# Optimization experiments

Hardware: AMD Instinct MI355X
Metric: run time of the kernel (lower is better)

The kernel has to match this reference:

```python
import jax, jax.numpy as jnp
import numpy as np

BN_EPS = 1e-5
NUM_GC_LAYERS = 3
NUM_LAYERS = NUM_GC_LAYERS + 4  # 7
N_NODES = 50000
N_EDGES = 600000
DIM = 128


def setup_inputs() -> dict:
    key = jax.random.key(0)
    ks = jax.random.split(key, 9)
    x = jax.random.normal(ks[0], (N_NODES, DIM), dtype=jnp.float32)
    edge_index = jax.random.randint(ks[1], (2, N_EDGES), 0, N_NODES, dtype=jnp.int64)
    batch = jnp.zeros((N_NODES,), dtype=jnp.int64)
    s = 0.1
    W1 = jax.random.normal(ks[2], (NUM_LAYERS, DIM, DIM), dtype=jnp.float32) * s
    b1 = jax.random.normal(ks[3], (NUM_LAYERS, DIM), dtype=jnp.float32) * s
    W2 = jax.random.normal(ks[4], (NUM_LAYERS, DIM, DIM), dtype=jnp.float32) * s
    b2 = jax.random.normal(ks[5], (NUM_LAYERS, DIM), dtype=jnp.float32) * s
    gamma = jnp.ones((NUM_LAYERS, DIM), dtype=jnp.float32)
    beta = jnp.zeros((NUM_LAYERS, DIM), dtype=jnp.float32)
    return {"x": x, "edge_index": edge_index, "batch": batch,
            "W1": W1, "b1": b1, "W2": W2, "b2": b2,
            "gamma": gamma, "beta": beta}


def _gin_conv(x, src, dst, W1, b1, W2, b2):
    # GINConv with eps=0: out = MLP(x + sum_{j in N(i)} x_j)
    agg = jax.ops.segment_sum(x[src], dst, num_segments=x.shape[0])  # [N, D]
    h = x + agg
    h = jnp.maximum(h @ W1 + b1, 0.0) @ W2 + b2
    return h


def _batch_norm(h, g, b):
    # BatchNorm1d in training mode: biased batch stats over nodes
    mean = jnp.mean(h, axis=0)
    var = jnp.var(h, axis=0)
    return (h - mean) * jax.lax.rsqrt(var + BN_EPS) * g + b


def reference(x, edge_index, batch, W1, b1, W2, b2, gamma, beta):
    src, dst = edge_index[0], edge_index[1]
    for i in range(NUM_GC_LAYERS):
        h = _gin_conv(x, src, dst, W1[i], b1[i], W2[i], b2[i])
        x = _batch_norm(jnp.maximum(h, 0.0), gamma[i], beta[i])
    j = NUM_GC_LAYERS
    outs = []
    for k in range(j, j + 4):
        h = _gin_conv(x, src, dst, W1[k], b1[k], W2[k], b2[k])
        outs.append(_batch_norm(jnp.tanh(h), gamma[k], beta[k]))
    return tuple(outs)
```

## Files before the change

### kernel.cpp

```cpp
#include <hip/hip_runtime.h>
#include <math.h>

#define NN 50000
#define NE 600000
#define DIM 128
#define NLAYERS 7
#define LDK 136
#define BN_EPS 1e-5f
#define GB 782
#define PART_SLOT 200192

typedef __attribute__((ext_vector_type(4))) float floatx4;
typedef __attribute__((ext_vector_type(8))) _Float16 half8;
typedef __attribute__((ext_vector_type(2))) _Float16 half2v;

__device__ __forceinline__ unsigned short f2h(float f) {
  _Float16 h = (_Float16)f;
  return __builtin_bit_cast(unsigned short, h);
}
__device__ __forceinline__ float2 up(unsigned int u) {
  half2v h = __builtin_bit_cast(half2v, u);
  return make_float2((float)h.x, (float)h.y);
}
__device__ __forceinline__ unsigned int pk(float a, float b) {
  half2v h;
  h.x = (_Float16)a;
  h.y = (_Float16)b;
  return __builtin_bit_cast(unsigned int, h);
}


__global__ void hist_kernel(const int* __restrict__ ei, int* __restrict__ deg) {
  int e = blockIdx.x * 256 + threadIdx.x;
  if (e < NE) atomicAdd(&deg[ei[NE + e]], 1);
}

__global__ __launch_bounds__(256) void scan_part(const int* __restrict__ deg,
                                                 int* __restrict__ rowl,
                                                 int* __restrict__ bsum) {
  int b = blockIdx.x, t = threadIdx.x;
  int base = b * 1024 + t * 4;
  int d[4];
  #pragma unroll
  for (int j = 0; j < 4; j++) d[j] = (base + j < NN) ? deg[base + j] : 0;
  int s = d[0] + d[1] + d[2] + d[3];
  int lane = t & 63;
  int incl = s;
  #pragma unroll
  for (int off = 1; off < 64; off <<= 1) {
    int n = __shfl_up(incl, off);
    if (lane >= off) incl += n;
  }
  __shared__ int wtot[4];
  if (lane == 63) wtot[t >> 6] = incl;
  __syncthreads();
  int woff = 0;
  for (int w = 0; w < (t >> 6); w++) woff += wtot[w];
  int run = woff + incl - s;
  #pragma unroll
  for (int j = 0; j < 4; j++) {
    if (base + j < NN) rowl[base + j] = run;
    run += d[j];
  }
  if (t == 255) bsum[b] = woff + incl;
}

__global__ void scan_top(const int* __restrict__ bsum, int* __restrict__ boff,
                         int* __restrict__ row) {
  int t = threadIdx.x;
  int v = (t < 49) ? bsum[t] : 0;
  int incl = v;
  #pragma unroll
  for (int off = 1; off < 64; off <<= 1) {
    int n = __shfl_up(incl, off);
    if (t >= off) incl += n;
  }
  if (t < 49) boff[t] = incl - v;
  if (t == 48) row[NN] = incl;
}

__global__ __launch_bounds__(256) void scan_apply(const int* __restrict__ rowl,
                                                  const int* __restrict__ boff,
                                                  int* __restrict__ row,
                                                  int* __restrict__ cur) {
  int i = blockIdx.x * 256 + threadIdx.x;
  if (i < NN) {
    int r = rowl[i] + boff[i >> 10];
    row[i] = r;
    cur[i] = r;
  }
}

__global__ void bucket_kernel(const int* __restrict__ ei, int* __restrict__ cur,
                              int* __restrict__ esrc) {
  int e = blockIdx.x * 256 + threadIdx.x;
  if (e < NE) {
    int d = ei[NE + e];
    int p = atomicAdd(&cur[d], 1);
    esrc[p] = ei[e];
  }
}


__global__ void convw_kernel(const float* __restrict__ W1, const float* __restrict__ W2,
                             unsigned short* __restrict__ wb) {
  int i = blockIdx.x * 256 + threadIdx.x;
  if (i >= NLAYERS * 16384) return;
  int l = i >> 14;
  int r = i & 16383;
  int n = r >> 7;
  int k = r & 127;
  wb[(size_t)(l * 2 + 0) * 16384 + n * 128 + k] = f2h(W1[(size_t)l * 16384 + k * 128 + n]);
  wb[(size_t)(l * 2 + 1) * 16384 + n * 128 + k] = f2h(W2[(size_t)l * 16384 + k * 128 + n]);
}

__global__ __launch_bounds__(256) void convx_kernel(const float* __restrict__ x,
                                                    unsigned int* __restrict__ x16) {
  int i = blockIdx.x * 256 + threadIdx.x;
  float4 v = ((const float4*)x)[i];
  uint2 o;
  o.x = pk(v.x, v.y);
  o.y = pk(v.z, v.w);
  ((uint2*)x16)[i] = o;
}


__global__ __launch_bounds__(256) void gather_kernel(
    const unsigned int* __restrict__ x16, const int* __restrict__ esrc,
    const int* __restrict__ row, unsigned int* __restrict__ agg16) {
  int w = (blockIdx.x * 256 + threadIdx.x) >> 6;
  int lane = threadIdx.x & 63;
  if (w >= NN) return;
  int s0 = row[w], s1 = row[w + 1];
  float ax = 0.f, ay = 0.f;
  int e = s0;
  for (; e + 3 < s1; e += 4) {
    int i0 = esrc[e], i1 = esrc[e + 1], i2 = esrc[e + 2], i3 = esrc[e + 3];
    unsigned int v0 = x16[i0 * 64 + lane];
    unsigned int v1 = x16[i1 * 64 + lane];
    unsigned int v2 = x16[i2 * 64 + lane];
    unsigned int v3 = x16[i3 * 64 + lane];
    float2 f0 = up(v0), f1 = up(v1), f2 = up(v2), f3 = up(v3);
    ax += (f0.x + f1.x) + (f2.x + f3.x);
    ay += (f0.y + f1.y) + (f2.y + f3.y);
  }
  for (; e < s1; e++) {
    float2 f = up(x16[esrc[e] * 64 + lane]);
    ax += f.x;
    ay += f.y;
  }
  agg16[w * 64 + lane] = pk(ax, ay);
}


__global__ __launch_bounds__(256) void mlp1_kernel(
    const unsigned int* __restrict__ x16, const unsigned int* __restrict__ agg16,
    const unsigned short* __restrict__ wb,
    const float* __restrict__ b1, const float* __restrict__ b2,
    unsigned short* __restrict__ xout16, float* __restrict__ part,
    const float* __restrict__ bnPrev, const float* __restrict__ gPrev,
    const float* __restrict__ btPrev, const int* __restrict__ deg, int hasPrev) {
  __shared__ unsigned short hS[64 * LDK];
  __shared__ unsigned short wS[128 * LDK];
  __shared__ float scshS[256];
  int tid = threadIdx.x;
  int row0 = blockIdx.x * 64;

  if (tid < 128) {
    float sc = 1.f, sh = 0.f;
    if (hasPrev) {
      const float inv = 1.f / (float)NN;
      float mean = bnPrev[tid] * inv;
      float var = bnPrev[128 + tid] * inv - mean * mean;
      sc = gPrev[tid] * rsqrtf(var + BN_EPS);
      sh = btPrev[tid] - mean * sc;
    }
    scshS[tid] = sc;
    scshS[128 + tid] = sh;
  }
  __syncthreads();

  for (int idx = tid; idx < 1024; idx += 256) {
    int r = idx >> 4;
    int c = (idx & 15) * 8;
    uint4 hv = {0u, 0u, 0u, 0u};
    if (row0 + r < NN) {
      size_t base = (size_t)(row0 + r) * 16 + (c >> 3);
      uint4 xv = ((const uint4*)x16)[base];
      uint4 av = ((const uint4*)agg16)[base];
      float dr = 1.f + (float)deg[row0 + r];
      unsigned int xs[4] = {xv.x, xv.y, xv.z, xv.w};
      unsigned int as_[4] = {av.x, av.y, av.z, av.w};
      unsigned int hs[4];
      #pragma unroll
      for (int j = 0; j < 4; j++) {
        float2 xf = up(xs[j]);
        float2 af = up(as_[j]);
        int cc = c + j * 2;
        float h0 = scshS[cc] * (xf.x + af.x) + dr * scshS[128 + cc];
        float h1 = scshS[cc + 1] * (xf.y + af.y) + dr * scshS[128 + cc + 1];
        hs[j] = pk(h0, h1);
      }
      hv.x = hs[0]; hv.y = hs[1]; hv.z = hs[2]; hv.w = hs[3];
    }
    *(uint4*)&hS[r * LDK + c] = hv;
  }
  for (int q = tid; q < 2048; q += 256) {
    int rw = q >> 4;
    int c8 = (q & 15) * 8;
    *(uint4*)&wS[rw * LDK + c8] = *(const uint4*)(wb + rw * 128 + c8);
  }
  __syncthreads();

  int lane = tid & 63;
  int wav = tid >> 6;
  int quad = lane >> 4;
  int lm = lane & 15;
  int mrow = wav * 16 + lm;

  floatx4 acc[8];
  #pragma unroll
  for (int nt = 0; nt < 8; nt++) {
    floatx4 c = {0.f, 0.f, 0.f, 0.f};
    #pragma unroll
    for (int ks = 0; ks < 4; ks++) {
      half8 af = *(half8*)&hS[mrow * LDK + ks * 32 + quad * 8];
      half8 bf = *(half8*)&wS[(nt * 16 + lm) * LDK + ks * 32 + quad * 8];
      c = __builtin_amdgcn_mfma_f32_16x16x32_f16(af, bf, c, 0, 0, 0);
    }
    acc[nt] = c;
  }
  #pragma unroll
  for (int nt = 0; nt < 8; nt++) {
    float bv = b1[nt * 16 + lm];
    #pragma unroll
    for (int rg = 0; rg < 4; rg++) {
      float v = acc[nt][rg] + bv;
      v = v > 0.f ? v : 0.f;
      hS[(wav * 16 + quad * 4 + rg) * LDK + nt * 16 + lm] = f2h(v);
    }
  }
  __syncthreads();
  for (int q = tid; q < 2048; q += 256) {
    int rw = q >> 4;
    int c8 = (q & 15) * 8;
    *(uint4*)&wS[rw * LDK + c8] = *(const uint4*)(wb + 16384 + rw * 128 + c8);
  }
  __syncthreads();

  bool wvalid = (row0 + wav * 16) < NN;
  float sArr[8], sqArr[8];
  #pragma unroll
  for (int nt = 0; nt < 8; nt++) {
    floatx4 c = {0.f, 0.f, 0.f, 0.f};
    #pragma unroll
    for (int ks = 0; ks < 4; ks++) {
      half8 af = *(half8*)&hS[mrow * LDK + ks * 32 + quad * 8];
      half8 bf = *(half8*)&wS[(nt * 16 + lm) * LDK + ks * 32 + quad * 8];
      c = __builtin_amdgcn_mfma_f32_16x16x32_f16(af, bf, c, 0, 0, 0);
    }
    float bv = b2[nt * 16 + lm];
    float s = 0.f, sq = 0.f;
    #pragma unroll
    for (int rg = 0; rg < 4; rg++) {
      float v = c[rg] + bv;
      v = v > 0.f ? v : 0.f;
      if (wvalid)
        xout16[(size_t)(row0 + wav * 16 + quad * 4 + rg) * DIM + nt * 16 + lm] = f2h(v);
      s += v;
      sq += v * v;
    }
    s += __shfl_xor(s, 16);
    s += __shfl_xor(s, 32);
    sq += __shfl_xor(sq, 16);
    sq += __shfl_xor(sq, 32);
    sArr[nt] = s;
    sqArr[nt] = sq;
  }
  __syncthreads();
  float* redS = (float*)hS;
  if (quad == 0) {
    #pragma unroll
    for (int nt = 0; nt < 8; nt++) {
      redS[wav * 256 + nt * 16 + lm] = wvalid ? sArr[nt] : 0.f;
      redS[wav * 256 + 128 + nt * 16 + lm] = wvalid ? sqArr[nt] : 0.f;
    }
  }
  __syncthreads();
  float v = redS[tid] + redS[256 + tid] + redS[512 + tid] + redS[768 + tid];
  part[(size_t)blockIdx.x * 256 + tid] = v;
}


__global__ __launch_bounds__(256) void mlp4_kernel(
    const unsigned int* __restrict__ x16, const unsigned int* __restrict__ agg16,
    const unsigned short* __restrict__ wbg,
    const float* __restrict__ b1g, const float* __restrict__ b2g,
    float* __restrict__ out, float* __restrict__ partBase,
    const float* __restrict__ bnPrev, const float* __restrict__ gPrev,
    const float* __restrict__ btPrev, const int* __restrict__ deg) {
  __shared__ unsigned short hS[64 * LDK];
  __shared__ unsigned short wS[128 * LDK];
  __shared__ float scshS[256];
  int tid = threadIdx.x;
  int row0 = blockIdx.x * 64;

  if (tid < 128) {
    const float inv = 1.f / (float)NN;
    float mean = bnPrev[tid] * inv;
    float var = bnPrev[128 + tid] * inv - mean * mean;
    float sc = gPrev[tid] * rsqrtf(var + BN_EPS);
    scshS[tid] = sc;
    scshS[128 + tid] = btPrev[tid] - mean * sc;
  }
  __syncthreads();

  for (int idx = tid; idx < 1024; idx += 256) {
    int r = idx >> 4;
    int c = (idx & 15) * 8;
    uint4 hv = {0u, 0u, 0u, 0u};
    if (row0 + r < NN) {
      size_t base = (size_t)(row0 + r) * 16 + (c >> 3);
      uint4 xv = ((const uint4*)x16)[base];
      uint4 av = ((const uint4*)agg16)[base];
      float dr = 1.f + (float)deg[row0 + r];
      unsigned int xs[4] = {xv.x, xv.y, xv.z, xv.w};
      unsigned int as_[4] = {av.x, av.y, av.z, av.w};
      unsigned int hs[4];
      #pragma unroll
      for (int j = 0; j < 4; j++) {
        float2 xf = up(xs[j]);
        float2 af = up(as_[j]);
        int cc = c + j * 2;
        float h0 = scshS[cc] * (xf.x + af.x) + dr * scshS[128 + cc];
        float h1 = scshS[cc + 1] * (xf.y + af.y) + dr * scshS[128 + cc + 1];
        hs[j] = pk(h0, h1);
      }
      hv.x = hs[0]; hv.y = hs[1]; hv.z = hs[2]; hv.w = hs[3];
    }
    *(uint4*)&hS[r * LDK + c] = hv;
  }
  __syncthreads();

  int lane = tid & 63;
  int wav = tid >> 6;
  int quad = lane >> 4;
  int lm = lane & 15;
  int mrow = wav * 16 + lm;
  bool wvalid = (row0 + wav * 16) < NN;

  half8 aF[4];
  #pragma unroll
  for (int ks = 0; ks < 4; ks++)
    aF[ks] = *(half8*)&hS[mrow * LDK + ks * 32 + quad * 8];

  #pragma unroll 1
  for (int ly = 0; ly < 4; ly++) {
    int layer = 3 + ly;
    const unsigned short* wb = wbg + (size_t)layer * 2 * 16384;
    const float* b1 = b1g + layer * 128;
    const float* b2 = b2g + layer * 128;
    float* act = out + (size_t)ly * NN * DIM;
    float* part = partBase + (size_t)ly * PART_SLOT;

    __syncthreads();
    for (int q = tid; q < 2048; q += 256) {
      int rw = q >> 4;
      int c8 = (q & 15) * 8;
      *(uint4*)&wS[rw * LDK + c8] = *(const uint4*)(wb + rw * 128 + c8);
    }
    __syncthreads();

    floatx4 acc[8];
    #pragma unroll
    for (int nt = 0; nt < 8; nt++) {
      floatx4 c = {0.f, 0.f, 0.f, 0.f};
      #pragma unroll
      for (int ks = 0; ks < 4; ks++) {
        half8 bf = *(half8*)&wS[(nt * 16 + lm) * LDK + ks * 32 + quad * 8];
        c = __builtin_amdgcn_mfma_f32_16x16x32_f16(aF[ks], bf, c, 0, 0, 0);
      }
      acc[nt] = c;
    }
    #pragma unroll
    for (int nt = 0; nt < 8; nt++) {
      float bv = b1[nt * 16 + lm];
      #pragma unroll
      for (int rg = 0; rg < 4; rg++) {
        float v = acc[nt][rg] + bv;
        v = v > 0.f ? v : 0.f;
        hS[(wav * 16 + quad * 4 + rg) * LDK + nt * 16 + lm] = f2h(v);
      }
    }
    __syncthreads();
    for (int q = tid; q < 2048; q += 256) {
      int rw = q >> 4;
      int c8 = (q & 15) * 8;
      *(uint4*)&wS[rw * LDK + c8] = *(const uint4*)(wb + 16384 + rw * 128 + c8);
    }
    __syncthreads();

    float sArr[8], sqArr[8];
    #pragma unroll
    for (int nt = 0; nt < 8; nt++) {
      floatx4 c = {0.f, 0.f, 0.f, 0.f};
      #pragma unroll
      for (int ks = 0; ks < 4; ks++) {
        half8 af = *(half8*)&hS[mrow * LDK + ks * 32 + quad * 8];
        half8 bf = *(half8*)&wS[(nt * 16 + lm) * LDK + ks * 32 + quad * 8];
        c = __builtin_amdgcn_mfma_f32_16x16x32_f16(af, bf, c, 0, 0, 0);
      }
      float bv = b2[nt * 16 + lm];
      float s = 0.f, sq = 0.f;
      #pragma unroll
      for (int rg = 0; rg < 4; rg++) {
        float v = c[rg] + bv;
        v = tanhf(v);
        if (wvalid)
          act[(size_t)(row0 + wav * 16 + quad * 4 + rg) * DIM + nt * 16 + lm] = v;
        s += v;
        sq += v * v;
      }
      s += __shfl_xor(s, 16);
      s += __shfl_xor(s, 32);
      sq += __shfl_xor(sq, 16);
      sq += __shfl_xor(sq, 32);
      sArr[nt] = s;
      sqArr[nt] = sq;
    }
    __syncthreads();
    float* redS = (float*)hS;
    if (quad == 0) {
      #pragma unroll
      for (int nt = 0; nt < 8; nt++) {
        redS[wav * 256 + nt * 16 + lm] = wvalid ? sArr[nt] : 0.f;
        redS[wav * 256 + 128 + nt * 16 + lm] = wvalid ? sqArr[nt] : 0.f;
      }
    }
    __syncthreads();
    float v = redS[tid] + redS[256 + tid] + redS[512 + tid] + redS[768 + tid];
    part[(size_t)blockIdx.x * 256 + tid] = v;
  }
}


__global__ __launch_bounds__(256) void reduce_kernel(const float* __restrict__ part,
                                                     float* __restrict__ bn) {
  int c = blockIdx.x;
  int t = threadIdx.x;
  const float* p = part + (size_t)blockIdx.y * PART_SLOT + c;
  float s = 0.f;
  for (int b = t; b < GB; b += 256) s += p[(size_t)b * 256];
  #pragma unroll
  for (int off = 1; off < 64; off <<= 1) s += __shfl_xor(s, off);
  __shared__ float wsum[4];
  if ((t & 63) == 0) wsum[t >> 6] = s;
  __syncthreads();
  if (t == 0) bn[blockIdx.y * 256 + c] = wsum[0] + wsum[1] + wsum[2] + wsum[3];
}


__global__ __launch_bounds__(256) void norm_kernel(
    const float* __restrict__ aBase, const float* __restrict__ bnAll,
    const float* __restrict__ gammaAll, const float* __restrict__ betaAll,
    float* __restrict__ oBase, int layer0) {
  int layer = layer0 + blockIdx.y;
  const float* a = aBase + (size_t)blockIdx.y * NN * DIM;
  const float* bn = bnAll + blockIdx.y * 256;
  const float* gamma = gammaAll + layer * 128;
  const float* beta = betaAll + layer * 128;
  float* o = oBase + (size_t)blockIdx.y * NN * DIM;
  int i = blockIdx.x * 256 + threadIdx.x;
  int f = (i & 31) * 4;
  const float inv = 1.f / (float)NN;
  float4 v = ((const float4*)a)[i];
  float r[4] = {v.x, v.y, v.z, v.w};
  #pragma unroll
  for (int j = 0; j < 4; j++) {
    float mean = bn[f + j] * inv;
    float var = bn[128 + f + j] * inv - mean * mean;
    float sc = gamma[f + j] * rsqrtf(var + BN_EPS);
    r[j] = (r[j] - mean) * sc + beta[f + j];
  }
  float4 ov; ov.x = r[0]; ov.y = r[1]; ov.z = r[2]; ov.w = r[3];
  ((float4*)o)[i] = ov;
}


extern "C" void kernel_launch(void* const* d_in, const int* in_sizes, int n_in,
                              void* d_out, int out_size, void* d_ws, size_t ws_size,
                              hipStream_t stream) {
  const float* x_in = (const float*)d_in[0];
  const int* ei = (const int*)d_in[1];
  const float* W1g = (const float*)d_in[3];
  const float* b1g = (const float*)d_in[4];
  const float* W2g = (const float*)d_in[5];
  const float* b2g = (const float*)d_in[6];
  const float* gg = (const float*)d_in[7];
  const float* bg = (const float*)d_in[8];
  float* out = (float*)d_out;

  char* ws = (char*)d_ws;
  const size_t OFF_X16 = 0;
  const size_t OFF_A16 = 12800000;
  const size_t OFF_WB = 25600000;
  const size_t OFF_BN = 26058752;
  const size_t OFF_DEG = 26062848;
  const size_t OFF_ROW = 26262848;
  const size_t OFF_CUR = 26462852;
  const size_t OFF_ESR = 26662852;
  const size_t OFF_PART = 29062852;

  unsigned int* X16 = (unsigned int*)(ws + OFF_X16);
  unsigned int* A16 = (unsigned int*)(ws + OFF_A16);
  unsigned short* wb = (unsigned short*)(ws + OFF_WB);
  float* bn = (float*)(ws + OFF_BN);
  int* deg = (int*)(ws + OFF_DEG);
  int* rowp = (int*)(ws + OFF_ROW);
  int* cur = (int*)(ws + OFF_CUR);
  int* esrc = (int*)(ws + OFF_ESR);
  float* part = (float*)(ws + OFF_PART);
  int* rowl = (int*)(ws + OFF_PART);
  int* bsum = (int*)(ws + OFF_PART + 800000);
  int* boff = (int*)(ws + OFF_PART + 800256);

  hipMemsetAsync(deg, 0, NN * sizeof(int), stream);
  hist_kernel<<<(NE + 255) / 256, 256, 0, stream>>>(ei, deg);
  scan_part<<<49, 256, 0, stream>>>(deg, rowl, bsum);
  scan_top<<<1, 64, 0, stream>>>(bsum, boff, rowp);
  scan_apply<<<196, 256, 0, stream>>>(rowl, boff, rowp, cur);
  bucket_kernel<<<(NE + 255) / 256, 256, 0, stream>>>(ei, cur, esrc);
  convw_kernel<<<(NLAYERS * 16384 + 255) / 256, 256, 0, stream>>>(W1g, W2g, wb);
  convx_kernel<<<NN * DIM / 4 / 256, 256, 0, stream>>>(x_in, X16);

  for (int i = 0; i < 3; i++) {
    gather_kernel<<<(NN * 64 + 255) / 256, 256, 0, stream>>>(X16, esrc, rowp, A16);
    mlp1_kernel<<<GB, 256, 0, stream>>>(
        X16, A16, wb + (size_t)i * 2 * 16384, b1g + i * 128, b2g + i * 128,
        (unsigned short*)X16, part,
        (i == 0) ? bn : bn + (i - 1) * 256,
        (i == 0) ? gg : gg + (i - 1) * 128,
        (i == 0) ? bg : bg + (i - 1) * 128, deg, i > 0 ? 1 : 0);
    reduce_kernel<<<dim3(256, 1), 256, 0, stream>>>(part, bn + i * 256);
  }
  gather_kernel<<<(NN * 64 + 255) / 256, 256, 0, stream>>>(X16, esrc, rowp, A16);
  mlp4_kernel<<<GB, 256, 0, stream>>>(X16, A16, wb, b1g, b2g, out, part,
                                      bn + 2 * 256, gg + 2 * 128, bg + 2 * 128, deg);
  reduce_kernel<<<dim3(256, 4), 256, 0, stream>>>(part, bn);
  norm_kernel<<<dim3(NN * DIM / 4 / 256, 4), 256, 0, stream>>>(out, bn, gg, bg, out, 3);
}
```

Baseline: 519.1 us.

## Bucket edges by source range, unify MLP kernel with swizzled LDS and split weights

Edges within each destination's CSR row are now sub-bucketed by source-node range (8 buckets), so gather reads walk source nodes in a more cache-local order. The MLP kernels merge into one templated kernel: LDS shrinks by loading weights in 64-row halves into an XOR-swizzled buffer, with register prefetch of the next half, and launch bounds request 4 blocks per CU. The four tanh layers run as a 2D grid instead of a serial loop in one block. A fast exp-based tanh replaces tanhf, trading some accuracy for speed.

```diff
diff --git a/kernel.cpp b/kernel.cpp
--- a/kernel.cpp
+++ b/kernel.cpp
@@ -5,7 +5,9 @@
 #define NE 600000
 #define DIM 128
 #define NLAYERS 7
-#define LDK 136
+#define NB 8
+#define NK (NN * NB)
+#define BDIV 6250
 #define BN_EPS 1e-5f
 #define GB 782
 #define PART_SLOT 200192
@@ -28,11 +30,22 @@
   h.y = (_Float16)b;
   return __builtin_bit_cast(unsigned int, h);
 }
-
-
-__global__ void hist_kernel(const int* __restrict__ ei, int* __restrict__ deg) {
+__device__ __forceinline__ float tanh_fast(float x) {
+  float e = __expf(2.0f * x);
+  return 1.0f - 2.0f * __builtin_amdgcn_rcpf(e + 1.0f);
+}
+__device__ __forceinline__ int hsw(int row, int scol) {
+  return row * 128 + (scol ^ ((row & 7) << 3));
+}
+
+
+__global__ void hist_kernel(const int* __restrict__ ei, int* __restrict__ deg2) {
   int e = blockIdx.x * 256 + threadIdx.x;
-  if (e < NE) atomicAdd(&deg[ei[NE + e]], 1);
+  if (e < NE) {
+    int d = ei[NE + e];
+    int s = ei[e];
+    atomicAdd(&deg2[d * NB + s / BDIV], 1);
+  }
 }
 
 __global__ __launch_bounds__(256) void scan_part(const int* __restrict__ deg,
@@ -42,7 +55,7 @@
   int base = b * 1024 + t * 4;
   int d[4];
   #pragma unroll
-  for (int j = 0; j < 4; j++) d[j] = (base + j < NN) ? deg[base + j] : 0;
+  for (int j = 0; j < 4; j++) d[j] = (base + j < NK) ? deg[base + j] : 0;
   int s = d[0] + d[1] + d[2] + d[3];
   int lane = t & 63;
   int incl = s;
@@ -59,36 +72,54 @@
   int run = woff + incl - s;
   #pragma unroll
   for (int j = 0; j < 4; j++) {
-    if (base + j < NN) rowl[base + j] = run;
+    if (base + j < NK) rowl[base + j] = run;
     run += d[j];
   }
   if (t == 255) bsum[b] = woff + incl;
 }
 
-__global__ void scan_top(const int* __restrict__ bsum, int* __restrict__ boff,
-                         int* __restrict__ row) {
+__global__ __launch_bounds__(256) void scan_top2(const int* __restrict__ bsum,
+                                                 int* __restrict__ boff,
+                                                 int* __restrict__ row2) {
+  const int nb = (NK + 1023) / 1024;
   int t = threadIdx.x;
-  int v = (t < 49) ? bsum[t] : 0;
-  int incl = v;
+  int v0 = (2 * t < nb) ? bsum[2 * t] : 0;
+  int v1 = (2 * t + 1 < nb) ? bsum[2 * t + 1] : 0;
+  int s = v0 + v1;
+  int lane = t & 63;
+  int incl = s;
   #pragma unroll
   for (int off = 1; off < 64; off <<= 1) {
     int n = __shfl_up(incl, off);
-    if (t >= off) incl += n;
-  }
-  if (t < 49) boff[t] = incl - v;
-  if (t == 48) row[NN] = incl;
+    if (lane >= off) incl += n;
+  }
+  __shared__ int wtot[4];
+  if (lane == 63) wtot[t >> 6] = incl;
+  __syncthreads();
+  int woff = 0;
+  for (int w = 0; w < (t >> 6); w++) woff += wtot[w];
+  int excl = woff + incl - s;
+  if (2 * t < nb) boff[2 * t] = excl;
+  if (2 * t + 1 < nb) boff[2 * t + 1] = excl + v0;
+  if (t == 255) row2[NK] = woff + incl;
 }
 
 __global__ __launch_bounds__(256) void scan_apply(const int* __restrict__ rowl,
                                                   const int* __restrict__ boff,
-                                                  int* __restrict__ row,
+                                                  int* __restrict__ row2,
                                                   int* __restrict__ cur) {
   int i = blockIdx.x * 256 + threadIdx.x;
-  if (i < NN) {
+  if (i < NK) {
     int r = rowl[i] + boff[i >> 10];
-    row[i] = r;
+    row2[i] = r;
     cur[i] = r;
   }
+}
+
+__global__ __launch_bounds__(256) void deg_kernel(const int* __restrict__ row2,
+                                                  int* __restrict__ deg) {
+  int i = blockIdx.x * 256 + threadIdx.x;
+  if (i < NN) deg[i] = row2[i * NB + NB] - row2[i * NB];
 }
 
 __global__ void bucket_kernel(const int* __restrict__ ei, int* __restrict__ cur,
@@ -96,8 +127,9 @@
   int e = blockIdx.x * 256 + threadIdx.x;
   if (e < NE) {
     int d = ei[NE + e];
-    int p = atomicAdd(&cur[d], 1);
-    esrc[p] = ei[e];
+    int s = ei[e];
+    int p = atomicAdd(&cur[d * NB + s / BDIV], 1);
+    esrc[p] = s;
   }
 }
 
@@ -131,7 +163,7 @@
   int w = (blockIdx.x * 256 + threadIdx.x) >> 6;
   int lane = threadIdx.x & 63;
   if (w >= NN) return;
-  int s0 = row[w], s1 = row[w + 1];
+  int s0 = row[w * NB], s1 = row[w * NB + NB];
   float ax = 0.f, ay = 0.f;
   int e = s0;
   for (; e + 3 < s1; e += 4) {
@@ -153,18 +185,28 @@
 }
 
 
-__global__ __launch_bounds__(256) void mlp1_kernel(
+template <int TANH>
+__global__ __launch_bounds__(256, 4) void mlp_kernel(
     const unsigned int* __restrict__ x16, const unsigned int* __restrict__ agg16,
     const unsigned short* __restrict__ wb,
     const float* __restrict__ b1, const float* __restrict__ b2,
-    unsigned short* __restrict__ xout16, float* __restrict__ part,
+    unsigned short* __restrict__ xout16, float* __restrict__ actout,
+    float* __restrict__ part,
     const float* __restrict__ bnPrev, const float* __restrict__ gPrev,
     const float* __restrict__ btPrev, const int* __restrict__ deg, int hasPrev) {
-  __shared__ unsigned short hS[64 * LDK];
-  __shared__ unsigned short wS[128 * LDK];
+  __shared__ unsigned short hS[64 * 128];
+  __shared__ unsigned short wS[64 * 128];
   __shared__ float scshS[256];
   int tid = threadIdx.x;
   int row0 = blockIdx.x * 64;
+  int lofs = TANH ? blockIdx.y : 0;
+  wb += (size_t)lofs * 32768;
+  b1 += lofs * 128;
+  b2 += lofs * 128;
+  if (TANH) {
+    actout += (size_t)lofs * NN * DIM;
+    part += (size_t)lofs * PART_SLOT;
+  }
 
   if (tid < 128) {
     float sc = 1.f, sh = 0.f;
@@ -178,37 +220,41 @@
     scshS[tid] = sc;
     scshS[128 + tid] = sh;
   }
-  __syncthreads();
-
-  for (int idx = tid; idx < 1024; idx += 256) {
+
+  uint4 wreg[4];
+  #pragma unroll
+  for (int j = 0; j < 4; j++) {
+    int q = tid + j * 256;
+    wreg[j] = *(const uint4*)(wb + (q >> 4) * 128 + (q & 15) * 8);
+  }
+  __syncthreads();
+
+  #pragma unroll
+  for (int j = 0; j < 4; j++) {
+    int idx = tid + j * 256;
     int r = idx >> 4;
     int c = (idx & 15) * 8;
     uint4 hv = {0u, 0u, 0u, 0u};
     if (row0 + r < NN) {
-      size_t base = (size_t)(row0 + r) * 16 + (c >> 3);
+      size_t base = (size_t)(row0 + r) * 16 + (idx & 15);
       uint4 xv = ((const uint4*)x16)[base];
       uint4 av = ((const uint4*)agg16)[base];
       float dr = 1.f + (float)deg[row0 + r];
       unsigned int xs[4] = {xv.x, xv.y, xv.z, xv.w};
       unsigned int as_[4] = {av.x, av.y, av.z, av.w};
-      unsigned int hs[4];
+      unsigned int hs4[4];
       #pragma unroll
-      for (int j = 0; j < 4; j++) {
-        float2 xf = up(xs[j]);
-        float2 af = up(as_[j]);
-        int cc = c + j * 2;
+      for (int jj = 0; jj < 4; jj++) {
+        float2 xf = up(xs[jj]);
+        float2 af = up(as_[jj]);
+        int cc = c + jj * 2;
         float h0 = scshS[cc] * (xf.x + af.x) + dr * scshS[128 + cc];
         float h1 = scshS[cc + 1] * (xf.y + af.y) + dr * scshS[128 + cc + 1];
-        hs[j] = pk(h0, h1);
+        hs4[jj] = pk(h0, h1);
       }
-      hv.x = hs[0]; hv.y = hs[1]; hv.z = hs[2]; hv.w = hs[3];
-    }
-    *(uint4*)&hS[r * LDK + c] = hv;
-  }
-  for (int q = tid; q < 2048; q += 256) {
-    int rw = q >> 4;
-    int c8 = (q & 15) * 8;
-    *(uint4*)&wS[rw * LDK + c8] = *(const uint4*)(wb + rw * 128 + c8);
+      hv.x = hs4[0]; hv.y = hs4[1]; hv.z = hs4[2]; hv.w = hs4[3];
+    }
+    *(uint4*)&hS[hsw(r, c)] = hv;
   }
   __syncthreads();
 
@@ -217,18 +263,57 @@
   int quad = lane >> 4;
   int lm = lane & 15;
   int mrow = wav * 16 + lm;
+  bool wvalid = (row0 + wav * 16) < NN;
+
+  half8 aF[4];
+  #pragma unroll
+  for (int ks = 0; ks < 4; ks++)
+    aF[ks] = *(half8*)&hS[hsw(mrow, ks * 32 + quad * 8)];
+
+  #pragma unroll
+  for (int j = 0; j < 4; j++) {
+    int q = tid + j * 256;
+    *(uint4*)&wS[hsw(q >> 4, (q & 15) * 8)] = wreg[j];
+  }
+  #pragma unroll
+  for (int j = 0; j < 4; j++) {
+    int q = tid + j * 256;
+    wreg[j] = *(const uint4*)(wb + 8192 + (q >> 4) * 128 + (q & 15) * 8);
+  }
+  __syncthreads();
 
   floatx4 acc[8];
   #pragma unroll
-  for (int nt = 0; nt < 8; nt++) {
-    floatx4 c = {0.f, 0.f, 0.f, 0.f};
+  for (int nt = 0; nt < 4; nt++) {
+    floatx4 cacc = {0.f, 0.f, 0.f, 0.f};
     #pragma unroll
     for (int ks = 0; ks < 4; ks++) {
-      half8 af = *(half8*)&hS[mrow * LDK + ks * 32 + quad * 8];
-      half8 bf = *(half8*)&wS[(nt * 16 + lm) * LDK + ks * 32 + quad * 8];
-      c = __builtin_amdgcn_mfma_f32_16x16x32_f16(af, bf, c, 0, 0, 0);
-    }
-    acc[nt] = c;
+      half8 bf = *(half8*)&wS[hsw(nt * 16 + lm, ks * 32 + quad * 8)];
+      cacc = __builtin_amdgcn_mfma_f32_16x16x32_f16(aF[ks], bf, cacc, 0, 0, 0);
+    }
+    acc[nt] = cacc;
+  }
+  __syncthreads();
+  #pragma unroll
+  for (int j = 0; j < 4; j++) {
+    int q = tid + j * 256;
+    *(uint4*)&wS[hsw(q >> 4, (q & 15) * 8)] = wreg[j];
+  }
+  #pragma unroll
+  for (int j = 0; j < 4; j++) {
+    int q = tid + j * 256;
+    wreg[j] = *(const uint4*)(wb + 16384 + (q >> 4) * 128 + (q & 15) * 8);
+  }
+  __syncthreads();
+  #pragma unroll
+  for (int nt = 4; nt < 8; nt++) {
+    floatx4 cacc = {0.f, 0.f, 0.f, 0.f};
+    #pragma unroll
+    for (int ks = 0; ks < 4; ks++) {
+      half8 bf = *(half8*)&wS[hsw((nt - 4) * 16 + lm, ks * 32 + quad * 8)];
+      cacc = __builtin_amdgcn_mfma_f32_16x16x32_f16(aF[ks], bf, cacc, 0, 0, 0);
+    }
+    acc[nt] = cacc;
   }
   #pragma unroll
   for (int nt = 0; nt < 8; nt++) {
@@ -237,36 +322,68 @@
     for (int rg = 0; rg < 4; rg++) {
       float v = acc[nt][rg] + bv;
       v = v > 0.f ? v : 0.f;
-      hS[(wav * 16 + quad * 4 + rg) * LDK + nt * 16 + lm] = f2h(v);
-    }
-  }
-  __syncthreads();
-  for (int q = tid; q < 2048; q += 256) {
-    int rw = q >> 4;
-    int c8 = (q & 15) * 8;
-    *(uint4*)&wS[rw * LDK + c8] = *(const uint4*)(wb + 16384 + rw * 128 + c8);
-  }
-  __syncthreads();
-
-  bool wvalid = (row0 + wav * 16) < NN;
+      hS[hsw(wav * 16 + quad * 4 + rg, nt * 16 + lm)] = f2h(v);
+    }
+  }
+  __syncthreads();
+  #pragma unroll
+  for (int j = 0; j < 4; j++) {
+    int q = tid + j * 256;
+    *(uint4*)&wS[hsw(q >> 4, (q & 15) * 8)] = wreg[j];
+  }
+  #pragma unroll
+  for (int j = 0; j < 4; j++) {
+    int q = tid + j * 256;
+    wreg[j] = *(const uint4*)(wb + 24576 + (q >> 4) * 128 + (q & 15) * 8);
+  }
+  __syncthreads();
+  half8 aG[4];
+  #pragma unroll
+  for (int ks = 0; ks < 4; ks++)
+    aG[ks] = *(half8*)&hS[hsw(mrow, ks * 32 + quad * 8)];
+  #pragma unroll
+  for (int nt = 0; nt < 4; nt++) {
+    floatx4 cacc = {0.f, 0.f, 0.f, 0.f};
+    #pragma unroll
+    for (int ks = 0; ks < 4; ks++) {
+      half8 bf = *(half8*)&wS[hsw(nt * 16 + lm, ks * 32 + quad * 8)];
+      cacc = __builtin_amdgcn_mfma_f32_16x16x32_f16(aG[ks], bf, cacc, 0, 0, 0);
+    }
+    acc[nt] = cacc;
+  }
+  __syncthreads();
+  #pragma unroll
+  for (int j = 0; j < 4; j++) {
+    int q = tid + j * 256;
+    *(uint4*)&wS[hsw(q >> 4, (q & 15) * 8)] = wreg[j];
+  }
+  __syncthreads();
+  #pragma unroll
+  for (int nt = 4; nt < 8; nt++) {
+    floatx4 cacc = {0.f, 0.f, 0.f, 0.f};
+    #pragma unroll
+    for (int ks = 0; ks < 4; ks++) {
+      half8 bf = *(half8*)&wS[hsw((nt - 4) * 16 + lm, ks * 32 + quad * 8)];
+      cacc = __builtin_amdgcn_mfma_f32_16x16x32_f16(aG[ks], bf, cacc, 0, 0, 0);
+    }
+    acc[nt] = cacc;
+  }
+
   float sArr[8], sqArr[8];
   #pragma unroll
   for (int nt = 0; nt < 8; nt++) {
-    floatx4 c = {0.f, 0.f, 0.f, 0.f};
-    #pragma unroll
-    for (int ks = 0; ks < 4; ks++) {
-      half8 af = *(half8*)&hS[mrow * LDK + ks * 32 + quad * 8];
-      half8 bf = *(half8*)&wS[(nt * 16 + lm) * LDK + ks * 32 + quad * 8];
-      c = __builtin_amdgcn_mfma_f32_16x16x32_f16(af, bf, c, 0, 0, 0);
-    }
     float bv = b2[nt * 16 + lm];
     float s = 0.f, sq = 0.f;
     #pragma unroll
     for (int rg = 0; rg < 4; rg++) {
-      float v = c[rg] + bv;
-      v = v > 0.f ? v : 0.f;
-      if (wvalid)
-        xout16[(size_t)(row0 + wav * 16 + quad * 4 + rg) * DIM + nt * 16 + lm] = f2h(v);
+      float v = acc[nt][rg] + bv;
+      if (TANH) v = tanh_fast(v);
+      else v = v > 0.f ? v : 0.f;
+      if (wvalid) {
+        size_t gi = (size_t)(row0 + wav * 16 + quad * 4 + rg) * DIM + nt * 16 + lm;
+        if (TANH) actout[gi] = v;
+        else xout16[gi] = f2h(v);
+      }
       s += v;
       sq += v * v;
     }
@@ -289,158 +406,6 @@
   __syncthreads();
   float v = redS[tid] + redS[256 + tid] + redS[512 + tid] + redS[768 + tid];
   part[(size_t)blockIdx.x * 256 + tid] = v;
-}
-
-
-__global__ __launch_bounds__(256) void mlp4_kernel(
-    const unsigned int* __restrict__ x16, const unsigned int* __restrict__ agg16,
-    const unsigned short* __restrict__ wbg,
-    const float* __restrict__ b1g, const float* __restrict__ b2g,
-    float* __restrict__ out, float* __restrict__ partBase,
-    const float* __restrict__ bnPrev, const float* __restrict__ gPrev,
-    const float* __restrict__ btPrev, const int* __restrict__ deg) {
-  __shared__ unsigned short hS[64 * LDK];
-  __shared__ unsigned short wS[128 * LDK];
-  __shared__ float scshS[256];
-  int tid = threadIdx.x;
-  int row0 = blockIdx.x * 64;
-
-  if (tid < 128) {
-    const float inv = 1.f / (float)NN;
-    float mean = bnPrev[tid] * inv;
-    float var = bnPrev[128 + tid] * inv - mean * mean;
-    float sc = gPrev[tid] * rsqrtf(var + BN_EPS);
-    scshS[tid] = sc;
-    scshS[128 + tid] = btPrev[tid] - mean * sc;
-  }
-  __syncthreads();
-
-  for (int idx = tid; idx < 1024; idx += 256) {
-    int r = idx >> 4;
-    int c = (idx & 15) * 8;
-    uint4 hv = {0u, 0u, 0u, 0u};
-    if (row0 + r < NN) {
-      size_t base = (size_t)(row0 + r) * 16 + (c >> 3);
-      uint4 xv = ((const uint4*)x16)[base];
-      uint4 av = ((const uint4*)agg16)[base];
-      float dr = 1.f + (float)deg[row0 + r];
-      unsigned int xs[4] = {xv.x, xv.y, xv.z, xv.w};
-      unsigned int as_[4] = {av.x, av.y, av.z, av.w};
-      unsigned int hs[4];
-      #pragma unroll
-      for (int j = 0; j < 4; j++) {
-        float2 xf = up(xs[j]);
-        float2 af = up(as_[j]);
-        int cc = c + j * 2;
-        float h0 = scshS[cc] * (xf.x + af.x) + dr * scshS[128 + cc];
-        float h1 = scshS[cc + 1] * (xf.y + af.y) + dr * scshS[128 + cc + 1];
-        hs[j] = pk(h0, h1);
-      }
-      hv.x = hs[0]; hv.y = hs[1]; hv.z = hs[2]; hv.w = hs[3];
-    }
-    *(uint4*)&hS[r * LDK + c] = hv;
-  }
-  __syncthreads();
-
-  int lane = tid & 63;
-  int wav = tid >> 6;
-  int quad = lane >> 4;
-  int lm = lane & 15;
-  int mrow = wav * 16 + lm;
-  bool wvalid = (row0 + wav * 16) < NN;
-
-  half8 aF[4];
-  #pragma unroll
-  for (int ks = 0; ks < 4; ks++)
-    aF[ks] = *(half8*)&hS[mrow * LDK + ks * 32 + quad * 8];
-
-  #pragma unroll 1
-  for (int ly = 0; ly < 4; ly++) {
-    int layer = 3 + ly;
-    const unsigned short* wb = wbg + (size_t)layer * 2 * 16384;
-    const float* b1 = b1g + layer * 128;
-    const float* b2 = b2g + layer * 128;
-    float* act = out + (size_t)ly * NN * DIM;
-    float* part = partBase + (size_t)ly * PART_SLOT;
-
-    __syncthreads();
-    for (int q = tid; q < 2048; q += 256) {
-      int rw = q >> 4;
-      int c8 = (q & 15) * 8;
-      *(uint4*)&wS[rw * LDK + c8] = *(const uint4*)(wb + rw * 128 + c8);
-    }
-    __syncthreads();
-
-    floatx4 acc[8];
-    #pragma unroll
-    for (int nt = 0; nt < 8; nt++) {
-      floatx4 c = {0.f, 0.f, 0.f, 0.f};
-      #pragma unroll
-      for (int ks = 0; ks < 4; ks++) {
-        half8 bf = *(half8*)&wS[(nt * 16 + lm) * LDK + ks * 32 + quad * 8];
-        c = __builtin_amdgcn_mfma_f32_16x16x32_f16(aF[ks], bf, c, 0, 0, 0);
-      }
-      acc[nt] = c;
-    }
-    #pragma unroll
-    for (int nt = 0; nt < 8; nt++) {
-      float bv = b1[nt * 16 + lm];
-      #pragma unroll
-      for (int rg = 0; rg < 4; rg++) {
-        float v = acc[nt][rg] + bv;
-        v = v > 0.f ? v : 0.f;
-        hS[(wav * 16 + quad * 4 + rg) * LDK + nt * 16 + lm] = f2h(v);
-      }
-    }
-    __syncthreads();
-    for (int q = tid; q < 2048; q += 256) {
-      int rw = q >> 4;
-      int c8 = (q & 15) * 8;
-      *(uint4*)&wS[rw * LDK + c8] = *(const uint4*)(wb + 16384 + rw * 128 + c8);
-    }
-    __syncthreads();
-
-    float sArr[8], sqArr[8];
-    #pragma unroll
-    for (int nt = 0; nt < 8; nt++) {
-      floatx4 c = {0.f, 0.f, 0.f, 0.f};
-      #pragma unroll
-      for (int ks = 0; ks < 4; ks++) {
-        half8 af = *(half8*)&hS[mrow * LDK + ks * 32 + quad * 8];
-        half8 bf = *(half8*)&wS[(nt * 16 + lm) * LDK + ks * 32 + quad * 8];
-        c = __builtin_amdgcn_mfma_f32_16x16x32_f16(af, bf, c, 0, 0, 0);
-      }
-      float bv = b2[nt * 16 + lm];
-      float s = 0.f, sq = 0.f;
-      #pragma unroll
-      for (int rg = 0; rg < 4; rg++) {
-        float v = c[rg] + bv;
-        v = tanhf(v);
-        if (wvalid)
-          act[(size_t)(row0 + wav * 16 + quad * 4 + rg) * DIM + nt * 16 + lm] = v;
-        s += v;
-        sq += v * v;
-      }
-      s += __shfl_xor(s, 16);
-      s += __shfl_xor(s, 32);
-      sq += __shfl_xor(sq, 16);
-      sq += __shfl_xor(sq, 32);
-      sArr[nt] = s;
-      sqArr[nt] = sq;
-    }
-    __syncthreads();
-    float* redS = (float*)hS;
-    if (quad == 0) {
-      #pragma unroll
-      for (int nt = 0; nt < 8; nt++) {
-        redS[wav * 256 + nt * 16 + lm] = wvalid ? sArr[nt] : 0.f;
-        redS[wav * 256 + 128 + nt * 16 + lm] = wvalid ? sqArr[nt] : 0.f;
-      }
-    }
-    __syncthreads();
-    float v = redS[tid] + redS[256 + tid] + redS[512 + tid] + redS[768 + tid];
-    part[(size_t)blockIdx.x * 256 + tid] = v;
-  }
 }
 
 
@@ -506,46 +471,47 @@
   const size_t OFF_WB = 25600000;
   const size_t OFF_BN = 26058752;
   const size_t OFF_DEG = 26062848;
-  const size_t OFF_ROW = 26262848;
-  const size_t OFF_CUR = 26462852;
-  const size_t OFF_ESR = 26662852;
-  const size_t OFF_PART = 29062852;
+  const size_t OFF_ROW2 = 26262848;
+  const size_t OFF_ESR = 27862864;
+  const size_t OFF_PART = 30262864;
 
   unsigned int* X16 = (unsigned int*)(ws + OFF_X16);
   unsigned int* A16 = (unsigned int*)(ws + OFF_A16);
   unsigned short* wb = (unsigned short*)(ws + OFF_WB);
   float* bn = (float*)(ws + OFF_BN);
   int* deg = (int*)(ws + OFF_DEG);
-  int* rowp = (int*)(ws + OFF_ROW);
-  int* cur = (int*)(ws + OFF_CUR);
+  int* row2 = (int*)(ws + OFF_ROW2);
   int* esrc = (int*)(ws + OFF_ESR);
   float* part = (float*)(ws + OFF_PART);
+  int* deg2 = (int*)(ws + OFF_A16);
   int* rowl = (int*)(ws + OFF_PART);
-  int* bsum = (int*)(ws + OFF_PART + 800000);
-  int* boff = (int*)(ws + OFF_PART + 800256);
-
-  hipMemsetAsync(deg, 0, NN * sizeof(int), stream);
-  hist_kernel<<<(NE + 255) / 256, 256, 0, stream>>>(ei, deg);
-  scan_part<<<49, 256, 0, stream>>>(deg, rowl, bsum);
-  scan_top<<<1, 64, 0, stream>>>(bsum, boff, rowp);
-  scan_apply<<<196, 256, 0, stream>>>(rowl, boff, rowp, cur);
-  bucket_kernel<<<(NE + 255) / 256, 256, 0, stream>>>(ei, cur, esrc);
+  int* bsum = (int*)(ws + OFF_PART + 1600000);
+  int* boff = (int*)(ws + OFF_PART + 1608000);
+
+  hipMemsetAsync(deg2, 0, NK * sizeof(int), stream);
+  hist_kernel<<<(NE + 255) / 256, 256, 0, stream>>>(ei, deg2);
+  scan_part<<<(NK + 1023) / 1024, 256, 0, stream>>>(deg2, rowl, bsum);
+  scan_top2<<<1, 256, 0, stream>>>(bsum, boff, row2);
+  scan_apply<<<(NK + 255) / 256, 256, 0, stream>>>(rowl, boff, row2, rowl);
+  deg_kernel<<<(NN + 255) / 256, 256, 0, stream>>>(row2, deg);
+  bucket_kernel<<<(NE + 255) / 256, 256, 0, stream>>>(ei, rowl, esrc);
   convw_kernel<<<(NLAYERS * 16384 + 255) / 256, 256, 0, stream>>>(W1g, W2g, wb);
   convx_kernel<<<NN * DIM / 4 / 256, 256, 0, stream>>>(x_in, X16);
 
   for (int i = 0; i < 3; i++) {
-    gather_kernel<<<(NN * 64 + 255) / 256, 256, 0, stream>>>(X16, esrc, rowp, A16);
-    mlp1_kernel<<<GB, 256, 0, stream>>>(
-        X16, A16, wb + (size_t)i * 2 * 16384, b1g + i * 128, b2g + i * 128,
-        (unsigned short*)X16, part,
+    gather_kernel<<<(NN * 64 + 255) / 256, 256, 0, stream>>>(X16, esrc, row2, A16);
+    mlp_kernel<0><<<GB, 256, 0, stream>>>(
+        X16, A16, wb + (size_t)i * 32768, b1g + i * 128, b2g + i * 128,
+        (unsigned short*)X16, nullptr, part,
         (i == 0) ? bn : bn + (i - 1) * 256,
         (i == 0) ? gg : gg + (i - 1) * 128,
         (i == 0) ? bg : bg + (i - 1) * 128, deg, i > 0 ? 1 : 0);
     reduce_kernel<<<dim3(256, 1), 256, 0, stream>>>(part, bn + i * 256);
   }
-  gather_kernel<<<(NN * 64 + 255) / 256, 256, 0, stream>>>(X16, esrc, rowp, A16);
-  mlp4_kernel<<<GB, 256, 0, stream>>>(X16, A16, wb, b1g, b2g, out, part,
-                                      bn + 2 * 256, gg + 2 * 128, bg + 2 * 128, deg);
+  gather_kernel<<<(NN * 64 + 255) / 256, 256, 0, stream>>>(X16, esrc, row2, A16);
+  mlp_kernel<1><<<dim3(GB, 4), 256, 0, stream>>>(
+      X16, A16, wb + 3 * 32768, b1g + 3 * 128, b2g + 3 * 128, nullptr, out, part,
+      bn + 2 * 256, gg + 2 * 128, bg + 2 * 128, deg, 1);
   reduce_kernel<<<dim3(256, 4), 256, 0, stream>>>(part, bn);
   norm_kernel<<<dim3(NN * DIM / 4 / 256, 4), 256, 0, stream>>>(out, bn, gg, bg, out, 3);
 }
```

Result: slower. 540.3 us (+4.1%).
